# Kernel tuning notes

Hardware: AMD Instinct MI355X
Metric: run time of the kernel (lower is better)

The kernel has to match this reference:

```python
import jax, jax.numpy as jnp
import numpy as np

B, C, CI, H, W = 8, 256, 128, 48, 48


def conv1x1(x, w, b):
    # x: (B,C,H,W), w: (CI,C), b: (CI,)
    return jnp.einsum('bchw,oc->bohw', x, w) + b[None, :, None, None]


def setup_inputs() -> dict:
    key = jax.random.key(0)
    ks = jax.random.split(key, 14)
    s = 1.0 / np.sqrt(C)
    d = {
        'x_1': jax.random.normal(ks[0], (B, C, H, W), jnp.float32),
        'x_2': jax.random.normal(ks[1], (B, C, H, W), jnp.float32),
    }
    names = ['v1', 'k1', 'q1', 'v2', 'k2', 'q2']
    for i, n in enumerate(names):
        d['w_' + n] = jax.random.uniform(ks[2 + 2 * i], (CI, C), jnp.float32, -s, s)
        d['b_' + n] = jax.random.uniform(ks[3 + 2 * i], (CI,), jnp.float32, -s, s)
    return d


def reference(x_1, x_2, w_v1, b_v1, w_k1, b_k1, w_q1, b_q1,
              w_v2, b_v2, w_k2, b_k2, w_q2, b_q2):
    b, ci, h, w = x_1.shape[0], w_v1.shape[0], x_1.shape[2], x_1.shape[3]
    n = h * w
    V1 = conv1x1(x_1, w_v1, b_v1).reshape(b, ci, n)
    K1 = conv1x1(x_1, w_k1, b_k1).reshape(b, ci, n)
    Q1 = conv1x1(x_1, w_q1, b_q1).reshape(b, ci, n)
    V2 = conv1x1(x_2, w_v2, b_v2).reshape(b, ci, n)
    K2 = conv1x1(x_2, w_k2, b_k2).reshape(b, ci, n)
    Q2 = conv1x1(x_2, w_q2, b_q2).reshape(b, ci, n)
    # sigmoid-gated cross attention, (B, N, N)
    R12 = jax.nn.sigmoid(jnp.einsum('bcn,bcm->bnm', Q1, K2))
    R21 = jax.nn.sigmoid(jnp.einsum('bcn,bcm->bnm', Q2, K1))
    Fu1 = jnp.einsum('bnm,bcm->bcn', R12, V2).reshape(b, ci, h, w)
    Fu2 = jnp.einsum('bnm,bcm->bcn', R21, V1).reshape(b, ci, h, w)
    y_1 = jnp.concatenate([x_1, Fu1], axis=1)
    y_2 = jnp.concatenate([x_2, Fu2], axis=1)
    return (y_1, y_2)
```

## Files before the change

### kernel.cpp

```cpp
#include <hip/hip_runtime.h>
#include <hip/hip_bf16.h>


typedef __bf16 bf16;
typedef __bf16 bf16x8 __attribute__((ext_vector_type(8)));
typedef __bf16 bf16x4 __attribute__((ext_vector_type(4)));
typedef float f32x4 __attribute__((ext_vector_type(4)));

#define NB 8
#define NC 256
#define NCI 128
#define NHW 2304
#define NT32 72
#define KPAD 136
#define VPAD 72

__global__ __launch_bounds__(256) void wconv_kernel(
    const float* __restrict__ w0, const float* __restrict__ w1,
    const float* __restrict__ w2, const float* __restrict__ w3,
    const float* __restrict__ w4, const float* __restrict__ w5,
    bf16* __restrict__ dst)
{
    int idx = (blockIdx.x * 256 + threadIdx.x) * 8;
    int m = idx >> 15;
    int off = idx & 32767;
    const float* w = (m == 0) ? w0 : (m == 1) ? w1 : (m == 2) ? w2
                   : (m == 3) ? w3 : (m == 4) ? w4 : w5;
    f32x4 a0 = *(const f32x4*)(w + off);
    f32x4 a1 = *(const f32x4*)(w + off + 4);
    bf16x8 o;
    #pragma unroll
    for (int j = 0; j < 4; ++j) { o[j] = (bf16)a0[j]; o[4 + j] = (bf16)a1[j]; }
    *(bf16x8*)(dst + idx) = o;
}

__global__ __launch_bounds__(256) void qkv_kernel(
    const float* __restrict__ x1, const float* __restrict__ x2,
    const bf16* __restrict__ wb,
    const float* __restrict__ bv1, const float* __restrict__ bk1, const float* __restrict__ bq1,
    const float* __restrict__ bv2, const float* __restrict__ bk2, const float* __restrict__ bq2,
    bf16* __restrict__ Qt, bf16* __restrict__ Kt, bf16* __restrict__ Vt,
    float* __restrict__ out)
{
    __shared__ __align__(16) bf16 Xt[32 * 264];

    int gid = blockIdx.x;
    int nt = gid % NT32;
    int s = (gid / NT32) & 1;
    int b = gid / (2 * NT32);
    int n0 = nt * 32;

    const float* x = s ? x2 : x1;
    const bf16* wv = wb + (size_t)(s * 3 + 0) * (NCI * NC);
    const bf16* wk = wb + (size_t)(s * 3 + 1) * (NCI * NC);
    const bf16* wq = wb + (size_t)(s * 3 + 2) * (NCI * NC);
    const float* bv = s ? bv2 : bv1;
    const float* bk = s ? bk2 : bk1;
    const float* bq = s ? bq2 : bq1;
    float* outy = out + (size_t)s * (NB * 384 * NHW);

    int tid = threadIdx.x;
    {
        int n_off = (tid & 3) * 8;
        int c0l = tid >> 2;
        #pragma unroll
        for (int i = 0; i < 4; ++i) {
            int c = c0l + i * 64;
            const float* src = x + ((size_t)(b * NC + c) * NHW + n0 + n_off);
            f32x4 a0 = *(const f32x4*)src;
            f32x4 a1 = *(const f32x4*)(src + 4);
            float* dsty = outy + ((size_t)(b * 384 + c) * NHW + n0 + n_off);
            *(f32x4*)dsty = a0;
            *(f32x4*)(dsty + 4) = a1;
            #pragma unroll
            for (int j = 0; j < 4; ++j) {
                Xt[(n_off + j) * 264 + c] = (bf16)a0[j];
                Xt[(n_off + 4 + j) * 264 + c] = (bf16)a1[j];
            }
        }
    }
    __syncthreads();

    int lane = tid & 63;
    int wid = tid >> 6;
    int row = lane & 15, quad = lane >> 4;
    int ci_base = wid * 32;

    f32x4 acc[3][2][2];
    #pragma unroll
    for (int t = 0; t < 3; ++t)
        #pragma unroll
        for (int mi = 0; mi < 2; ++mi)
            #pragma unroll
            for (int j = 0; j < 2; ++j)
                acc[t][mi][j] = (f32x4){0.f, 0.f, 0.f, 0.f};

    const bf16* wptr[3] = {wq, wk, wv};
    #pragma unroll
    for (int ks = 0; ks < 8; ++ks) {
        int c0 = ks * 32 + quad * 8;
        bf16x8 bfrag[2];
        #pragma unroll
        for (int j = 0; j < 2; ++j)
            bfrag[j] = *(const bf16x8*)&Xt[(j * 16 + row) * 264 + c0];
        #pragma unroll
        for (int t = 0; t < 3; ++t) {
            #pragma unroll
            for (int mi = 0; mi < 2; ++mi) {
                bf16x8 afrag = *(const bf16x8*)&wptr[t][(size_t)(ci_base + mi * 16 + row) * NC + c0];
                #pragma unroll
                for (int j = 0; j < 2; ++j)
                    acc[t][mi][j] = __builtin_amdgcn_mfma_f32_16x16x32_bf16(
                        afrag, bfrag[j], acc[t][mi][j], 0, 0, 0);
            }
        }
    }

    size_t qkbase = ((size_t)s * NB + b) * NHW * NCI;
    size_t vbase  = ((size_t)s * NB + b) * NCI * NHW;
    #pragma unroll
    for (int mi = 0; mi < 2; ++mi) {
        int ci0 = ci_base + mi * 16 + quad * 4;
        f32x4 bq4 = *(const f32x4*)&bq[ci0];
        f32x4 bk4 = *(const f32x4*)&bk[ci0];
        f32x4 bv4 = *(const f32x4*)&bv[ci0];
        #pragma unroll
        for (int j = 0; j < 2; ++j) {
            int n = n0 + j * 16 + row;
            bf16x4 pk;
            #pragma unroll
            for (int r = 0; r < 4; ++r) pk[r] = (bf16)(acc[0][mi][j][r] + bq4[r]);
            *(bf16x4*)&Qt[qkbase + (size_t)n * NCI + ci0] = pk;
            #pragma unroll
            for (int r = 0; r < 4; ++r) pk[r] = (bf16)(acc[1][mi][j][r] + bk4[r]);
            *(bf16x4*)&Kt[qkbase + (size_t)n * NCI + ci0] = pk;
            #pragma unroll
            for (int r = 0; r < 4; ++r)
                Vt[vbase + (size_t)(ci0 + r) * NHW + n] = (bf16)(acc[2][mi][j][r] + bv4[r]);
        }
    }
}

__global__ __launch_bounds__(256) void attn_kernel(
    const bf16* __restrict__ Qt, const bf16* __restrict__ Kt, const bf16* __restrict__ Vt,
    float* __restrict__ out)
{
    __shared__ __align__(16) bf16 KT[64 * KPAD];
    __shared__ __align__(16) bf16 VT[128 * VPAD];
    __shared__ __align__(16) bf16 P[4][16 * 72];

    int gid = blockIdx.x;
    int pair = (gid & 7) * 2 + ((gid >> 3) & 1);
    int nt = gid >> 4;
    int dir = pair & 1;
    int b = pair >> 1;
    int n0 = nt * 64;

    int tid = threadIdx.x;
    int lane = tid & 63, w = tid >> 6;
    int row = lane & 15, quad = lane >> 4;

    int sq = dir, skv = dir ^ 1;
    const bf16* q = Qt + ((size_t)sq  * NB + b) * (NHW * NCI);
    const bf16* k = Kt + ((size_t)skv * NB + b) * (NHW * NCI);
    const bf16* v = Vt + ((size_t)skv * NB + b) * (NCI * NHW);
    float* outy = out + (size_t)dir * (NB * 384 * NHW) + ((size_t)b * 384 + 256) * NHW;

    int kgoff[4], vgoff[4];
    bf16 *klp[4], *vlp[4];
    #pragma unroll
    for (int i = 0; i < 4; ++i) {
        int c = tid + i * 256;
        int kr = c >> 4, kc = c & 15;
        kgoff[i] = kr * NCI + kc * 8;
        klp[i] = &KT[kr * KPAD + kc * 8];
        int vr = c >> 3, vc = c & 7;
        vgoff[i] = vr * NHW + vc * 8;
        vlp[i] = &VT[vr * VPAD + vc * 8];
    }

    int nw = n0 + w * 16;
    bf16x8 qf[4];
    #pragma unroll
    for (int ks = 0; ks < 4; ++ks)
        qf[ks] = *(const bf16x8*)&q[(size_t)(nw + row) * NCI + ks * 32 + quad * 8];

    f32x4 o[8];
    #pragma unroll
    for (int ct = 0; ct < 8; ++ct) o[ct] = (f32x4){0.f, 0.f, 0.f, 0.f};

    bf16* Pw = P[w];

    bf16x8 kreg[4], vreg[4];
    #pragma unroll
    for (int i = 0; i < 4; ++i) {
        kreg[i] = *(const bf16x8*)(k + kgoff[i]);
        vreg[i] = *(const bf16x8*)(v + vgoff[i]);
    }

    for (int mt = 0; mt < 36; ++mt) {
        __syncthreads();
        #pragma unroll
        for (int i = 0; i < 4; ++i) {
            *(bf16x8*)klp[i] = kreg[i];
            *(bf16x8*)vlp[i] = vreg[i];
        }
        __syncthreads();
        if (mt < 35) {
            size_t ko = (size_t)(mt + 1) * 64 * NCI;
            int vo = (mt + 1) * 64;
            #pragma unroll
            for (int i = 0; i < 4; ++i) {
                kreg[i] = *(const bf16x8*)(k + ko + kgoff[i]);
                vreg[i] = *(const bf16x8*)(v + vo + vgoff[i]);
            }
        }
        f32x4 sacc[4];
        #pragma unroll
        for (int j = 0; j < 4; ++j) sacc[j] = (f32x4){0.f, 0.f, 0.f, 0.f};
        #pragma unroll
        for (int ks = 0; ks < 4; ++ks) {
            #pragma unroll
            for (int j = 0; j < 4; ++j) {
                bf16x8 kf = *(const bf16x8*)&KT[(j * 16 + row) * KPAD + ks * 32 + quad * 8];
                sacc[j] = __builtin_amdgcn_mfma_f32_16x16x32_bf16(qf[ks], kf, sacc[j], 0, 0, 0);
            }
        }
        #pragma unroll
        for (int j = 0; j < 4; ++j) {
            #pragma unroll
            for (int r = 0; r < 4; ++r) {
                float xv = sacc[j][r];
                float e = __expf(-xv);
                float p = __builtin_amdgcn_rcpf(1.0f + e);
                Pw[(quad * 4 + r) * 72 + j * 16 + row] = (bf16)p;
            }
        }
        #pragma unroll
        for (int ks = 0; ks < 2; ++ks) {
            bf16x8 af = *(const bf16x8*)&Pw[row * 72 + ks * 32 + quad * 8];
            #pragma unroll
            for (int ct = 0; ct < 8; ++ct) {
                bf16x8 vf = *(const bf16x8*)&VT[(ct * 16 + row) * VPAD + ks * 32 + quad * 8];
                o[ct] = __builtin_amdgcn_mfma_f32_16x16x32_bf16(af, vf, o[ct], 0, 0, 0);
            }
        }
    }

    int nbase = nw + quad * 4;
    #pragma unroll
    for (int ct = 0; ct < 8; ++ct) {
        int c = ct * 16 + row;
        *(f32x4*)&outy[(size_t)c * NHW + nbase] = o[ct];
    }
}

extern "C" void kernel_launch(void* const* d_in, const int* in_sizes, int n_in,
                              void* d_out, int out_size, void* d_ws, size_t ws_size,
                              hipStream_t stream) {
    const float* x1  = (const float*)d_in[0];
    const float* x2  = (const float*)d_in[1];
    const float* wv1 = (const float*)d_in[2];  const float* bv1 = (const float*)d_in[3];
    const float* wk1 = (const float*)d_in[4];  const float* bk1 = (const float*)d_in[5];
    const float* wq1 = (const float*)d_in[6];  const float* bq1 = (const float*)d_in[7];
    const float* wv2 = (const float*)d_in[8];  const float* bv2 = (const float*)d_in[9];
    const float* wk2 = (const float*)d_in[10]; const float* bk2 = (const float*)d_in[11];
    const float* wq2 = (const float*)d_in[12]; const float* bq2 = (const float*)d_in[13];
    float* out = (float*)d_out;

    size_t per = (size_t)2 * NB * NHW * NCI;
    bf16* Qt = (bf16*)d_ws;
    bf16* Kt = Qt + per;
    bf16* Vt = Kt + per;
    bf16* wb = Vt + per;

    wconv_kernel<<<dim3(96), dim3(256), 0, stream>>>(wv1, wk1, wq1, wv2, wk2, wq2, wb);

    qkv_kernel<<<dim3(NB * 2 * NT32), dim3(256), 0, stream>>>(
        x1, x2, wb, bv1, bk1, bq1, bv2, bk2, bq2, Qt, Kt, Vt, out);

    attn_kernel<<<dim3(NB * 2 * 36), dim3(256), 0, stream>>>(Qt, Kt, Vt, out);
}
```

Baseline: 251.6 us.

## Rework attention kernel with 32x32 MFMA, split-KV waves, register P path

Rewrites the attention kernel to use 32x32x16 bf16 MFMAs, with the 4 waves split into 2 query sub-tiles and 2 KV halves, and the two halves reduced through LDS at the end. The sigmoid probabilities stay in registers via v_cvt_pk_bf16 and v_permlane32_swap instead of a round trip through LDS. The padded LDS layouts are replaced by XOR swizzles, and s_setprio is set around the MFMA blocks. The goal is to cut LDS traffic and raise matrix-core throughput per instruction, at the cost of more register pressure (launch_bounds 256,2), a final cross-wave reduction step, and stores in the epilogue that are no longer vectorised.

```diff
diff --git a/kernel.cpp b/kernel.cpp
--- a/kernel.cpp
+++ b/kernel.cpp
@@ -6,14 +6,13 @@
 typedef __bf16 bf16x8 __attribute__((ext_vector_type(8)));
 typedef __bf16 bf16x4 __attribute__((ext_vector_type(4)));
 typedef float f32x4 __attribute__((ext_vector_type(4)));
+typedef float f32x16 __attribute__((ext_vector_type(16)));
 
 #define NB 8
 #define NC 256
 #define NCI 128
 #define NHW 2304
 #define NT32 72
-#define KPAD 136
-#define VPAD 72
 
 __global__ __launch_bounds__(256) void wconv_kernel(
     const float* __restrict__ w0, const float* __restrict__ w1,
@@ -141,24 +140,26 @@
     }
 }
 
-__global__ __launch_bounds__(256) void attn_kernel(
+__global__ __launch_bounds__(256, 2) void attn_kernel(
     const bf16* __restrict__ Qt, const bf16* __restrict__ Kt, const bf16* __restrict__ Vt,
     float* __restrict__ out)
 {
-    __shared__ __align__(16) bf16 KT[64 * KPAD];
-    __shared__ __align__(16) bf16 VT[128 * VPAD];
-    __shared__ __align__(16) bf16 P[4][16 * 72];
+    __shared__ __align__(16) bf16 KH[2 * 64 * 128];
+    __shared__ __align__(16) bf16 VH[2 * 128 * 64];
 
     int gid = blockIdx.x;
     int pair = (gid & 7) * 2 + ((gid >> 3) & 1);
-    int nt = gid >> 4;
+    int nb = gid >> 4;
     int dir = pair & 1;
     int b = pair >> 1;
-    int n0 = nt * 64;
 
     int tid = threadIdx.x;
-    int lane = tid & 63, w = tid >> 6;
-    int row = lane & 15, quad = lane >> 4;
+    int lane = tid & 63;
+    int w = tid >> 6;
+    int ns = w & 1;
+    int mh = w >> 1;
+    int col = lane & 31;
+    int hi = lane >> 5;
 
     int sq = dir, skv = dir ^ 1;
     const bf16* q = Qt + ((size_t)sq  * NB + b) * (NHW * NCI);
@@ -166,92 +167,157 @@
     const bf16* v = Vt + ((size_t)skv * NB + b) * (NCI * NHW);
     float* outy = out + (size_t)dir * (NB * 384 * NHW) + ((size_t)b * 384 + 256) * NHW;
 
-    int kgoff[4], vgoff[4];
-    bf16 *klp[4], *vlp[4];
+    int kgoff[4], vgoff[4], kloff[4], vloff[4];
     #pragma unroll
     for (int i = 0; i < 4; ++i) {
         int c = tid + i * 256;
         int kr = c >> 4, kc = c & 15;
         kgoff[i] = kr * NCI + kc * 8;
-        klp[i] = &KT[kr * KPAD + kc * 8];
+        kloff[i] = kr * 128 + ((kc ^ (kr & 15)) * 8);
         int vr = c >> 3, vc = c & 7;
         vgoff[i] = vr * NHW + vc * 8;
-        vlp[i] = &VT[vr * VPAD + vc * 8];
-    }
-
-    int nw = n0 + w * 16;
-    bf16x8 qf[4];
-    #pragma unroll
-    for (int ks = 0; ks < 4; ++ks)
-        qf[ks] = *(const bf16x8*)&q[(size_t)(nw + row) * NCI + ks * 32 + quad * 8];
-
-    f32x4 o[8];
-    #pragma unroll
-    for (int ct = 0; ct < 8; ++ct) o[ct] = (f32x4){0.f, 0.f, 0.f, 0.f};
-
-    bf16* Pw = P[w];
-
-    bf16x8 kreg[4], vreg[4];
-    #pragma unroll
-    for (int i = 0; i < 4; ++i) {
-        kreg[i] = *(const bf16x8*)(k + kgoff[i]);
-        vreg[i] = *(const bf16x8*)(v + vgoff[i]);
-    }
-
-    for (int mt = 0; mt < 36; ++mt) {
+        vloff[i] = vr * 64 + ((vc ^ (vr & 7)) * 8);
+    }
+
+    int nw = nb * 64 + ns * 32;
+    bf16x8 qf[8];
+    #pragma unroll
+    for (int kq = 0; kq < 8; ++kq)
+        qf[kq] = *(const bf16x8*)&q[(size_t)(nw + col) * NCI + kq * 16 + hi * 8];
+
+    f32x16 o[4];
+    #pragma unroll
+    for (int ct = 0; ct < 4; ++ct)
+        #pragma unroll
+        for (int j = 0; j < 16; ++j) o[ct][j] = 0.f;
+
+    bf16x8 rk[2][4], rv[2][4];
+    #pragma unroll
+    for (int h = 0; h < 2; ++h) {
+        const bf16* kp = k + (size_t)(h * 1152) * NCI;
+        const bf16* vp = v + h * 1152;
+        #pragma unroll
+        for (int i = 0; i < 4; ++i) {
+            rk[h][i] = *(const bf16x8*)(kp + kgoff[i]);
+            rv[h][i] = *(const bf16x8*)(vp + vgoff[i]);
+        }
+    }
+
+    const bf16* KB = &KH[mh * (64 * 128)];
+    const bf16* VB = &VH[mh * (128 * 64)];
+
+    for (int it = 0; it < 18; ++it) {
         __syncthreads();
         #pragma unroll
-        for (int i = 0; i < 4; ++i) {
-            *(bf16x8*)klp[i] = kreg[i];
-            *(bf16x8*)vlp[i] = vreg[i];
-        }
+        for (int h = 0; h < 2; ++h)
+            #pragma unroll
+            for (int i = 0; i < 4; ++i) {
+                *(bf16x8*)&KH[h * (64 * 128) + kloff[i]] = rk[h][i];
+                *(bf16x8*)&VH[h * (128 * 64) + vloff[i]] = rv[h][i];
+            }
         __syncthreads();
-        if (mt < 35) {
-            size_t ko = (size_t)(mt + 1) * 64 * NCI;
-            int vo = (mt + 1) * 64;
-            #pragma unroll
-            for (int i = 0; i < 4; ++i) {
-                kreg[i] = *(const bf16x8*)(k + ko + kgoff[i]);
-                vreg[i] = *(const bf16x8*)(v + vo + vgoff[i]);
-            }
-        }
-        f32x4 sacc[4];
-        #pragma unroll
-        for (int j = 0; j < 4; ++j) sacc[j] = (f32x4){0.f, 0.f, 0.f, 0.f};
-        #pragma unroll
-        for (int ks = 0; ks < 4; ++ks) {
-            #pragma unroll
-            for (int j = 0; j < 4; ++j) {
-                bf16x8 kf = *(const bf16x8*)&KT[(j * 16 + row) * KPAD + ks * 32 + quad * 8];
-                sacc[j] = __builtin_amdgcn_mfma_f32_16x16x32_bf16(qf[ks], kf, sacc[j], 0, 0, 0);
-            }
-        }
-        #pragma unroll
-        for (int j = 0; j < 4; ++j) {
-            #pragma unroll
-            for (int r = 0; r < 4; ++r) {
-                float xv = sacc[j][r];
-                float e = __expf(-xv);
-                float p = __builtin_amdgcn_rcpf(1.0f + e);
-                Pw[(quad * 4 + r) * 72 + j * 16 + row] = (bf16)p;
-            }
-        }
-        #pragma unroll
-        for (int ks = 0; ks < 2; ++ks) {
-            bf16x8 af = *(const bf16x8*)&Pw[row * 72 + ks * 32 + quad * 8];
-            #pragma unroll
-            for (int ct = 0; ct < 8; ++ct) {
-                bf16x8 vf = *(const bf16x8*)&VT[(ct * 16 + row) * VPAD + ks * 32 + quad * 8];
-                o[ct] = __builtin_amdgcn_mfma_f32_16x16x32_bf16(af, vf, o[ct], 0, 0, 0);
-            }
-        }
-    }
-
-    int nbase = nw + quad * 4;
-    #pragma unroll
-    for (int ct = 0; ct < 8; ++ct) {
-        int c = ct * 16 + row;
-        *(f32x4*)&outy[(size_t)c * NHW + nbase] = o[ct];
+        if (it < 17) {
+            #pragma unroll
+            for (int h = 0; h < 2; ++h) {
+                const bf16* kp = k + (size_t)(h * 1152 + (it + 1) * 64) * NCI;
+                const bf16* vp = v + (h * 1152 + (it + 1) * 64);
+                #pragma unroll
+                for (int i = 0; i < 4; ++i) {
+                    rk[h][i] = *(const bf16x8*)(kp + kgoff[i]);
+                    rv[h][i] = *(const bf16x8*)(vp + vgoff[i]);
+                }
+            }
+        }
+
+        f32x16 s0, s1;
+        #pragma unroll
+        for (int j = 0; j < 16; ++j) { s0[j] = 0.f; s1[j] = 0.f; }
+
+        __builtin_amdgcn_s_setprio(1);
+        #pragma unroll
+        for (int kq = 0; kq < 8; ++kq) {
+            bf16x8 kf0 = *(const bf16x8*)&KB[col * 128 + (((2 * kq + hi) ^ (col & 15)) * 8)];
+            s0 = __builtin_amdgcn_mfma_f32_32x32x16_bf16(kf0, qf[kq], s0, 0, 0, 0);
+            bf16x8 kf1 = *(const bf16x8*)&KB[(32 + col) * 128 + (((2 * kq + hi) ^ (col & 15)) * 8)];
+            s1 = __builtin_amdgcn_mfma_f32_32x32x16_bf16(kf1, qf[kq], s1, 0, 0, 0);
+        }
+        __builtin_amdgcn_s_setprio(0);
+
+        union PBu { unsigned int u[4]; bf16x8 v; };
+        PBu pb[4];
+        #pragma unroll
+        for (int ms = 0; ms < 2; ++ms) {
+            float p[16];
+            #pragma unroll
+            for (int r = 0; r < 16; ++r) {
+                float sv = (ms == 0) ? s0[r] : s1[r];
+                float e = __expf(-sv);
+                p[r] = __builtin_amdgcn_rcpf(1.0f + e);
+            }
+            #pragma unroll
+            for (int kst = 0; kst < 2; ++kst) {
+                unsigned int a0, a1, b0, b1;
+                asm("v_cvt_pk_bf16_f32 %0, %1, %2" : "=v"(a0) : "v"(p[8*kst+0]), "v"(p[8*kst+1]));
+                asm("v_cvt_pk_bf16_f32 %0, %1, %2" : "=v"(a1) : "v"(p[8*kst+2]), "v"(p[8*kst+3]));
+                asm("v_cvt_pk_bf16_f32 %0, %1, %2" : "=v"(b0) : "v"(p[8*kst+4]), "v"(p[8*kst+5]));
+                asm("v_cvt_pk_bf16_f32 %0, %1, %2" : "=v"(b1) : "v"(p[8*kst+6]), "v"(p[8*kst+7]));
+                asm volatile("v_permlane32_swap_b32 %0, %1" : "+v"(a0), "+v"(b0));
+                asm volatile("v_permlane32_swap_b32 %0, %1" : "+v"(a1), "+v"(b1));
+                pb[ms * 2 + kst].u[0] = a0;
+                pb[ms * 2 + kst].u[1] = a1;
+                pb[ms * 2 + kst].u[2] = b0;
+                pb[ms * 2 + kst].u[3] = b1;
+            }
+        }
+
+        __builtin_amdgcn_s_setprio(1);
+        #pragma unroll
+        for (int km = 0; km < 4; ++km) {
+            #pragma unroll
+            for (int ct = 0; ct < 4; ++ct) {
+                bf16x8 vf = *(const bf16x8*)&VB[(ct * 32 + col) * 64 + (((2 * km + hi) ^ (col & 7)) * 8)];
+                o[ct] = __builtin_amdgcn_mfma_f32_32x32x16_bf16(vf, pb[km].v, o[ct], 0, 0, 0);
+            }
+        }
+        __builtin_amdgcn_s_setprio(0);
+    }
+
+    __syncthreads();
+    float* RED = (float*)KH;
+    {
+        float* buf = RED + (ns * 2 + mh) * 2048;
+        int cb = (mh ^ 1) * 2;
+        #pragma unroll
+        for (int ci = 0; ci < 2; ++ci)
+            #pragma unroll
+            for (int g = 0; g < 4; ++g) {
+                f32x4 val;
+                #pragma unroll
+                for (int j = 0; j < 4; ++j) val[j] = o[cb + ci][g * 4 + j];
+                *(f32x4*)&buf[lane * 32 + (((ci * 4 + g) ^ (lane & 7)) * 4)] = val;
+            }
+    }
+    __syncthreads();
+    {
+        float* buf = RED + (ns * 2 + (mh ^ 1)) * 2048;
+        int cb = mh * 2;
+        #pragma unroll
+        for (int ci = 0; ci < 2; ++ci)
+            #pragma unroll
+            for (int g = 0; g < 4; ++g) {
+                f32x4 val = *(const f32x4*)&buf[lane * 32 + (((ci * 4 + g) ^ (lane & 7)) * 4)];
+                #pragma unroll
+                for (int j = 0; j < 4; ++j) o[cb + ci][g * 4 + j] += val[j];
+            }
+        #pragma unroll
+        for (int ci = 0; ci < 2; ++ci) {
+            int ct = cb + ci;
+            #pragma unroll
+            for (int r = 0; r < 16; ++r) {
+                int c = ct * 32 + (r & 3) + 8 * (r >> 2) + 4 * hi;
+                outy[(size_t)c * NHW + nw + col] = o[ct][r];
+            }
+        }
     }
 }
 
```

Measured after the change: 403.5 us. 1.6x slower.

## Split attention KV range across waves with 32x32 MFMA and LDS reduction

Applied to the files above, without the earlier changes.

Rewrites the attention kernel so each block handles 32 query rows. Its four waves each cover a quarter of the key/value range, loading K and V fragments straight from global memory instead of staging them through shared memory. It uses 32x32x16 MFMAs, keeps P in registers via packed bf16 conversion and permlane32 swaps, and combines the per-wave partial outputs with a swizzled LDS reduction. V is written by the projection kernel in a tiled 32-column layout so it can be read directly. This removes the per-tile barriers and LDS traffic and doubles grid size for occupancy, at the cost of more redundant global/L2 reads of K/V and a final reduction step.

```diff
diff --git a/kernel.cpp b/kernel.cpp
--- a/kernel.cpp
+++ b/kernel.cpp
@@ -6,14 +6,14 @@
 typedef __bf16 bf16x8 __attribute__((ext_vector_type(8)));
 typedef __bf16 bf16x4 __attribute__((ext_vector_type(4)));
 typedef float f32x4 __attribute__((ext_vector_type(4)));
+typedef float f32x16 __attribute__((ext_vector_type(16)));
+typedef unsigned int u32x4 __attribute__((ext_vector_type(4)));
 
 #define NB 8
 #define NC 256
 #define NCI 128
 #define NHW 2304
 #define NT32 72
-#define KPAD 136
-#define VPAD 72
 
 __global__ __launch_bounds__(256) void wconv_kernel(
     const float* __restrict__ w0, const float* __restrict__ w1,
@@ -136,29 +136,27 @@
             *(bf16x4*)&Kt[qkbase + (size_t)n * NCI + ci0] = pk;
             #pragma unroll
             for (int r = 0; r < 4; ++r)
-                Vt[vbase + (size_t)(ci0 + r) * NHW + n] = (bf16)(acc[2][mi][j][r] + bv4[r]);
+                Vt[vbase + (size_t)(nt * 128 + ci0 + r) * 32 + (j * 16 + row)] =
+                    (bf16)(acc[2][mi][j][r] + bv4[r]);
         }
     }
 }
 
-__global__ __launch_bounds__(256) void attn_kernel(
+__global__ __launch_bounds__(256, 3) void attn_kernel(
     const bf16* __restrict__ Qt, const bf16* __restrict__ Kt, const bf16* __restrict__ Vt,
     float* __restrict__ out)
 {
-    __shared__ __align__(16) bf16 KT[64 * KPAD];
-    __shared__ __align__(16) bf16 VT[128 * VPAD];
-    __shared__ __align__(16) bf16 P[4][16 * 72];
+    __shared__ __align__(16) float RED[8192];
 
     int gid = blockIdx.x;
-    int pair = (gid & 7) * 2 + ((gid >> 3) & 1);
+    int b = gid & 7;
+    int dir = (gid >> 3) & 1;
     int nt = gid >> 4;
-    int dir = pair & 1;
-    int b = pair >> 1;
-    int n0 = nt * 64;
 
     int tid = threadIdx.x;
-    int lane = tid & 63, w = tid >> 6;
-    int row = lane & 15, quad = lane >> 4;
+    int lane = tid & 63;
+    int mq = tid >> 6;
+    int col = lane & 31, hi = lane >> 5;
 
     int sq = dir, skv = dir ^ 1;
     const bf16* q = Qt + ((size_t)sq  * NB + b) * (NHW * NCI);
@@ -166,92 +164,118 @@
     const bf16* v = Vt + ((size_t)skv * NB + b) * (NCI * NHW);
     float* outy = out + (size_t)dir * (NB * 384 * NHW) + ((size_t)b * 384 + 256) * NHW;
 
-    int kgoff[4], vgoff[4];
-    bf16 *klp[4], *vlp[4];
-    #pragma unroll
-    for (int i = 0; i < 4; ++i) {
-        int c = tid + i * 256;
-        int kr = c >> 4, kc = c & 15;
-        kgoff[i] = kr * NCI + kc * 8;
-        klp[i] = &KT[kr * KPAD + kc * 8];
-        int vr = c >> 3, vc = c & 7;
-        vgoff[i] = vr * NHW + vc * 8;
-        vlp[i] = &VT[vr * VPAD + vc * 8];
-    }
-
-    int nw = n0 + w * 16;
-    bf16x8 qf[4];
-    #pragma unroll
-    for (int ks = 0; ks < 4; ++ks)
-        qf[ks] = *(const bf16x8*)&q[(size_t)(nw + row) * NCI + ks * 32 + quad * 8];
-
-    f32x4 o[8];
-    #pragma unroll
-    for (int ct = 0; ct < 8; ++ct) o[ct] = (f32x4){0.f, 0.f, 0.f, 0.f};
-
-    bf16* Pw = P[w];
-
-    bf16x8 kreg[4], vreg[4];
-    #pragma unroll
-    for (int i = 0; i < 4; ++i) {
-        kreg[i] = *(const bf16x8*)(k + kgoff[i]);
-        vreg[i] = *(const bf16x8*)(v + vgoff[i]);
-    }
-
-    for (int mt = 0; mt < 36; ++mt) {
-        __syncthreads();
-        #pragma unroll
-        for (int i = 0; i < 4; ++i) {
-            *(bf16x8*)klp[i] = kreg[i];
-            *(bf16x8*)vlp[i] = vreg[i];
-        }
-        __syncthreads();
-        if (mt < 35) {
-            size_t ko = (size_t)(mt + 1) * 64 * NCI;
-            int vo = (mt + 1) * 64;
-            #pragma unroll
-            for (int i = 0; i < 4; ++i) {
-                kreg[i] = *(const bf16x8*)(k + ko + kgoff[i]);
-                vreg[i] = *(const bf16x8*)(v + vo + vgoff[i]);
-            }
-        }
-        f32x4 sacc[4];
-        #pragma unroll
-        for (int j = 0; j < 4; ++j) sacc[j] = (f32x4){0.f, 0.f, 0.f, 0.f};
-        #pragma unroll
-        for (int ks = 0; ks < 4; ++ks) {
-            #pragma unroll
-            for (int j = 0; j < 4; ++j) {
-                bf16x8 kf = *(const bf16x8*)&KT[(j * 16 + row) * KPAD + ks * 32 + quad * 8];
-                sacc[j] = __builtin_amdgcn_mfma_f32_16x16x32_bf16(qf[ks], kf, sacc[j], 0, 0, 0);
-            }
-        }
-        #pragma unroll
-        for (int j = 0; j < 4; ++j) {
-            #pragma unroll
-            for (int r = 0; r < 4; ++r) {
-                float xv = sacc[j][r];
-                float e = __expf(-xv);
-                float p = __builtin_amdgcn_rcpf(1.0f + e);
-                Pw[(quad * 4 + r) * 72 + j * 16 + row] = (bf16)p;
-            }
-        }
-        #pragma unroll
-        for (int ks = 0; ks < 2; ++ks) {
-            bf16x8 af = *(const bf16x8*)&Pw[row * 72 + ks * 32 + quad * 8];
-            #pragma unroll
-            for (int ct = 0; ct < 8; ++ct) {
-                bf16x8 vf = *(const bf16x8*)&VT[(ct * 16 + row) * VPAD + ks * 32 + quad * 8];
-                o[ct] = __builtin_amdgcn_mfma_f32_16x16x32_bf16(af, vf, o[ct], 0, 0, 0);
-            }
-        }
-    }
-
-    int nbase = nw + quad * 4;
-    #pragma unroll
-    for (int ct = 0; ct < 8; ++ct) {
-        int c = ct * 16 + row;
-        *(f32x4*)&outy[(size_t)c * NHW + nbase] = o[ct];
+    int nw = nt * 32;
+
+    bf16x8 qf[8];
+    #pragma unroll
+    for (int j = 0; j < 8; ++j)
+        qf[j] = *(const bf16x8*)&q[(size_t)(nw + col) * NCI + j * 16 + hi * 8];
+
+    f32x16 o0, o1, o2, o3;
+    #pragma unroll
+    for (int j = 0; j < 16; ++j) { o0[j] = 0.f; o1[j] = 0.f; o2[j] = 0.f; o3[j] = 0.f; }
+
+    for (int i = 0; i < 18; ++i) {
+        int m0 = mq * 576 + i * 32;
+        const bf16* kp = k + (size_t)(m0 + col) * NCI + hi * 8;
+
+        f32x16 s;
+        #pragma unroll
+        for (int j = 0; j < 16; ++j) s[j] = 0.f;
+        __builtin_amdgcn_s_setprio(1);
+        #pragma unroll
+        for (int j = 0; j < 8; ++j) {
+            bf16x8 kf = *(const bf16x8*)(kp + j * 16);
+            s = __builtin_amdgcn_mfma_f32_32x32x16_bf16(kf, qf[j], s, 0, 0, 0);
+        }
+        __builtin_amdgcn_s_setprio(0);
+
+        #pragma unroll
+        for (int r = 0; r < 16; ++r) {
+            float e = __expf(-s[r]);
+            s[r] = __builtin_amdgcn_rcpf(1.0f + e);
+        }
+        u32x4 pbw0, pbw1;
+        {
+            unsigned int a0, a1, c0, c1;
+            asm("v_cvt_pk_bf16_f32 %0, %1, %2" : "=v"(a0) : "v"(s[0]), "v"(s[1]));
+            asm("v_cvt_pk_bf16_f32 %0, %1, %2" : "=v"(a1) : "v"(s[2]), "v"(s[3]));
+            asm("v_cvt_pk_bf16_f32 %0, %1, %2" : "=v"(c0) : "v"(s[4]), "v"(s[5]));
+            asm("v_cvt_pk_bf16_f32 %0, %1, %2" : "=v"(c1) : "v"(s[6]), "v"(s[7]));
+            asm volatile("v_permlane32_swap_b32 %0, %1" : "+v"(a0), "+v"(c0));
+            asm volatile("v_permlane32_swap_b32 %0, %1" : "+v"(a1), "+v"(c1));
+            pbw0 = (u32x4){a0, a1, c0, c1};
+        }
+        {
+            unsigned int a0, a1, c0, c1;
+            asm("v_cvt_pk_bf16_f32 %0, %1, %2" : "=v"(a0) : "v"(s[8]),  "v"(s[9]));
+            asm("v_cvt_pk_bf16_f32 %0, %1, %2" : "=v"(a1) : "v"(s[10]), "v"(s[11]));
+            asm("v_cvt_pk_bf16_f32 %0, %1, %2" : "=v"(c0) : "v"(s[12]), "v"(s[13]));
+            asm("v_cvt_pk_bf16_f32 %0, %1, %2" : "=v"(c1) : "v"(s[14]), "v"(s[15]));
+            asm volatile("v_permlane32_swap_b32 %0, %1" : "+v"(a0), "+v"(c0));
+            asm volatile("v_permlane32_swap_b32 %0, %1" : "+v"(a1), "+v"(c1));
+            pbw1 = (u32x4){a0, a1, c0, c1};
+        }
+
+        const bf16* vp = v + ((size_t)(mq * 18 + i) * 128 + col) * 32 + hi * 8;
+        __builtin_amdgcn_s_setprio(1);
+        {
+            bf16x8 pf = __builtin_bit_cast(bf16x8, pbw0);
+            o0 = __builtin_amdgcn_mfma_f32_32x32x16_bf16(*(const bf16x8*)(vp + 0*1024), pf, o0, 0, 0, 0);
+            o1 = __builtin_amdgcn_mfma_f32_32x32x16_bf16(*(const bf16x8*)(vp + 1*1024), pf, o1, 0, 0, 0);
+            o2 = __builtin_amdgcn_mfma_f32_32x32x16_bf16(*(const bf16x8*)(vp + 2*1024), pf, o2, 0, 0, 0);
+            o3 = __builtin_amdgcn_mfma_f32_32x32x16_bf16(*(const bf16x8*)(vp + 3*1024), pf, o3, 0, 0, 0);
+        }
+        {
+            bf16x8 pf = __builtin_bit_cast(bf16x8, pbw1);
+            o0 = __builtin_amdgcn_mfma_f32_32x32x16_bf16(*(const bf16x8*)(vp + 0*1024 + 16), pf, o0, 0, 0, 0);
+            o1 = __builtin_amdgcn_mfma_f32_32x32x16_bf16(*(const bf16x8*)(vp + 1*1024 + 16), pf, o1, 0, 0, 0);
+            o2 = __builtin_amdgcn_mfma_f32_32x32x16_bf16(*(const bf16x8*)(vp + 2*1024 + 16), pf, o2, 0, 0, 0);
+            o3 = __builtin_amdgcn_mfma_f32_32x32x16_bf16(*(const bf16x8*)(vp + 3*1024 + 16), pf, o3, 0, 0, 0);
+        }
+        __builtin_amdgcn_s_setprio(0);
+    }
+
+    float* buf0 = RED;
+    float* buf1 = RED + 4096;
+
+    auto wpart = [&](float* buf, const f32x16& a, int cb) {
+        #pragma unroll
+        for (int g = 0; g < 4; ++g) {
+            f32x4 v4;
+            #pragma unroll
+            for (int j = 0; j < 4; ++j) v4[j] = a[g * 4 + j];
+            *(f32x4*)&buf[lane * 64 + (((cb * 4 + g) ^ (lane & 15)) * 4)] = v4;
+        }
+    };
+    auto rpart = [&](float* buf, f32x16& a, int cb) {
+        #pragma unroll
+        for (int g = 0; g < 4; ++g) {
+            f32x4 v4 = *(const f32x4*)&buf[lane * 64 + (((cb * 4 + g) ^ (lane & 15)) * 4)];
+            #pragma unroll
+            for (int j = 0; j < 4; ++j) a[g * 4 + j] += v4[j];
+        }
+    };
+
+    __syncthreads();
+    if (mq == 2) { wpart(buf0, o0, 0); wpart(buf0, o1, 1); wpart(buf0, o2, 2); wpart(buf0, o3, 3); }
+    if (mq == 3) { wpart(buf1, o0, 0); wpart(buf1, o1, 1); wpart(buf1, o2, 2); wpart(buf1, o3, 3); }
+    __syncthreads();
+    if (mq == 0) { rpart(buf0, o0, 0); rpart(buf0, o1, 1); rpart(buf0, o2, 2); rpart(buf0, o3, 3); }
+    if (mq == 1) { rpart(buf1, o0, 0); rpart(buf1, o1, 1); rpart(buf1, o2, 2); rpart(buf1, o3, 3); }
+    __syncthreads();
+    if (mq == 1) { wpart(buf0, o0, 0); wpart(buf0, o1, 1); wpart(buf0, o2, 2); wpart(buf0, o3, 3); }
+    __syncthreads();
+    if (mq == 0) {
+        rpart(buf0, o0, 0); rpart(buf0, o1, 1); rpart(buf0, o2, 2); rpart(buf0, o3, 3);
+        #pragma unroll
+        for (int r = 0; r < 16; ++r) {
+            int cr = (r & 3) + 8 * (r >> 2) + 4 * hi;
+            outy[(size_t)(0 * 32 + cr) * NHW + nw + col] = o0[r];
+            outy[(size_t)(1 * 32 + cr) * NHW + nw + col] = o1[r];
+            outy[(size_t)(2 * 32 + cr) * NHW + nw + col] = o2[r];
+            outy[(size_t)(3 * 32 + cr) * NHW + nw + col] = o3[r];
+        }
     }
 }
 
@@ -279,5 +303,5 @@
     qkv_kernel<<<dim3(NB * 2 * NT32), dim3(256), 0, stream>>>(
         x1, x2, wb, bv1, bk1, bq1, bv2, bk2, bq2, Qt, Kt, Vt, out);
 
-    attn_kernel<<<dim3(NB * 2 * 36), dim3(256), 0, stream>>>(Qt, Kt, Vt, out);
+    attn_kernel<<<dim3(NB * 2 * NT32), dim3(256), 0, stream>>>(Qt, Kt, Vt, out);
 }
```

New measurement: 288.9 us. +14.8%, slower.
